# Performance work log

Hardware: AMD Instinct MI355X
Metric: run time of the kernel (lower is better)

The kernel has to match this reference:

```python
import jax, jax.numpy as jnp
import numpy as np

D_MODEL = 192   # embed_dim
DEPTH = 24
D_INNER = 384   # expand=2 * d_model
D_STATE = 16
D_CONV = 4
DT_RANK = 12    # ceil(192/16)
B = 8
IMG = 224
P = 16          # patch size / stride


def setup_inputs() -> dict:
    key = jax.random.key(0)
    ks = jax.random.split(key, 10)
    s = lambda k, shp, sc=0.02: jax.random.normal(k, shp, jnp.float32) * sc
    return {
        "x": jax.random.normal(ks[0], (B, 3, IMG, IMG), jnp.float32),
        "pe_w": s(ks[1], (D_MODEL, 3, P, P)),
        "pe_b": jnp.zeros((D_MODEL,), jnp.float32),
        "norm_w": jnp.ones((DEPTH, D_MODEL), jnp.float32),
        "norm_b": jnp.zeros((DEPTH, D_MODEL), jnp.float32),
        "in_proj_w": s(ks[2], (DEPTH, 2 * D_INNER, D_MODEL)),
        "conv_w": s(ks[3], (DEPTH, D_INNER, D_CONV), 0.1),
        "conv_b": jnp.zeros((DEPTH, D_INNER), jnp.float32),
        "xproj_w": s(ks[4], (DEPTH, DT_RANK + 2 * D_STATE, D_INNER)),
        "dtproj_w": s(ks[5], (DEPTH, D_INNER, DT_RANK), 0.1),
        "dtproj_b": s(ks[6], (DEPTH, D_INNER), 0.1),
        "A_log": jnp.broadcast_to(jnp.log(jnp.arange(1.0, D_STATE + 1.0, dtype=jnp.float32)), (DEPTH, D_INNER, D_STATE)).astype(jnp.float32),
        "D_param": jnp.ones((DEPTH, D_INNER), jnp.float32),
        "outproj_w": s(ks[7], (DEPTH, D_MODEL, D_INNER)),
        "normf_w": jnp.ones((D_MODEL,), jnp.float32),
        "normf_b": jnp.zeros((D_MODEL,), jnp.float32),
    }


def _layernorm(x, w, b, eps=1e-5):
    mu = x.mean(-1, keepdims=True)
    var = ((x - mu) ** 2).mean(-1, keepdims=True)
    return (x - mu) * jax.lax.rsqrt(var + eps) * w + b


def _causal_dwconv(x, w, b):
    # x: [B, L, d_inner]; depthwise causal conv1d (mamba conv1d, padding=d_conv-1, truncated to L)
    xt = jnp.pad(x.swapaxes(1, 2), ((0, 0), (0, 0), (D_CONV - 1, 0)))  # [B, di, L+3]
    y = jax.lax.conv_general_dilated(xt, w[:, None, :], (1,), 'VALID',
                                     feature_group_count=w.shape[0])
    return (y + b[:, None]).swapaxes(1, 2)  # [B, L, di]


def _selective_scan(u, dt, Bm, Cm, A, Dp):
    # u, dt: [B, L, di]; Bm, Cm: [B, L, ds]; A: [di, ds]; Dp: [di]
    dA = jnp.exp(dt[..., None] * A)                         # [B, L, di, ds]
    dBu = (dt * u)[..., None] * Bm[:, :, None, :]           # [B, L, di, ds]

    def step(h, inp):
        dA_t, dBu_t, C_t = inp
        h = dA_t * h + dBu_t                                # [B, di, ds]
        return h, jnp.einsum('bds,bs->bd', h, C_t)

    h0 = jnp.zeros((u.shape[0], A.shape[0], A.shape[1]), u.dtype)
    _, ys = jax.lax.scan(step, h0,
                         (dA.swapaxes(0, 1), dBu.swapaxes(0, 1), Cm.swapaxes(0, 1)))
    return ys.swapaxes(0, 1) + u * Dp                       # [B, L, di]


def _mamba(x, ipw, cw, cb, xpw, dtw, dtb, Alog, Dp, opw):
    xz = jnp.einsum('bld,ed->ble', x, ipw)                  # [B, L, 2*di]
    xin, z = jnp.split(xz, 2, axis=-1)
    xin = jax.nn.silu(_causal_dwconv(xin, cw, cb))
    xdbl = jnp.einsum('bld,ed->ble', xin, xpw)              # [B, L, dt_rank+2*ds]
    dt = jax.nn.softplus(jnp.einsum('blr,dr->bld', xdbl[..., :DT_RANK], dtw) + dtb)
    Bm = xdbl[..., DT_RANK:DT_RANK + D_STATE]
    Cm = xdbl[..., DT_RANK + D_STATE:]
    A = -jnp.exp(Alog)
    y = _selective_scan(xin, dt, Bm, Cm, A, Dp)
    y = y * jax.nn.silu(z)
    return jnp.einsum('bld,ed->ble', y, opw)                # [B, L, D]


def reference(x, pe_w, pe_b, norm_w, norm_b, in_proj_w, conv_w, conv_b,
              xproj_w, dtproj_w, dtproj_b, A_log, D_param, outproj_w,
              normf_w, normf_b):
    # PatchEmbed: conv stride 16 -> flatten -> [B, 196, 192]
    feat = jax.lax.conv_general_dilated(x, pe_w, (P, P), 'VALID') + pe_b[None, :, None, None]
    h = feat.reshape(feat.shape[0], D_MODEL, -1).swapaxes(1, 2)
    residual = None
    for i in range(DEPTH):
        residual = h if residual is None else residual + h
        hn = _layernorm(residual, norm_w[i], norm_b[i])
        h = _mamba(hn, in_proj_w[i], conv_w[i], conv_b[i], xproj_w[i],
                   dtproj_w[i], dtproj_b[i], A_log[i], D_param[i], outproj_w[i])
    residual = residual + h
    return _layernorm(residual, normf_w, normf_b)           # [B, 196, 192]
```

## Files before the change

### kernel.cpp

```cpp
#include <hip/hip_runtime.h>
#include <hip/hip_bf16.h>


#define NTOK   1568
#define DMODEL 192
#define DINNER 384
#define DSTATE 16
#define DTRANK 12
#define DEPTH  24
#define LSEQ   196
#define TCH    49
#define LDA    40

typedef __attribute__((ext_vector_type(8))) short short8;
typedef __attribute__((ext_vector_type(4))) short short4v;
typedef __attribute__((ext_vector_type(4))) float floatx4;

__device__ inline short f2bf(float f) {
    __hip_bfloat16 h = __float2bfloat16(f);
    return *reinterpret_cast<short*>(&h);
}

#define PR1 884736
#define PR2 1327104
#define PR3 1363968
#define PR4 1769472
#define PR5 1880064
#define PR6 3084288
__global__ __launch_bounds__(256) void prep(
    const float* __restrict__ inw, const float* __restrict__ outw,
    const float* __restrict__ pew, const float* __restrict__ xpw,
    const float* __restrict__ dtw, const float* __restrict__ x,
    short* __restrict__ w_in, short* __restrict__ w_out,
    short* __restrict__ w_pe, float* __restrict__ xpwT,
    float* __restrict__ dtwT, __hip_bfloat16* __restrict__ patches)
{
    int idx = blockIdx.x * 256 + threadIdx.x;
    if (idx < PR3) {
        float4 v; short* dst;
        if (idx < PR1)      { v = ((const float4*)inw)[idx];        dst = w_in  + (size_t)idx * 4; }
        else if (idx < PR2) { int i = idx - PR1; v = ((const float4*)outw)[i]; dst = w_out + (size_t)i * 4; }
        else                { int i = idx - PR2; v = ((const float4*)pew)[i];  dst = w_pe  + (size_t)i * 4; }
        short4v o;
        o[0] = f2bf(v.x); o[1] = f2bf(v.y); o[2] = f2bf(v.z); o[3] = f2bf(v.w);
        *(short4v*)dst = o;
    } else if (idx < PR4) {
        int i = idx - PR3;
        int layer = i / 16896, rem = i % 16896;
        int k = rem / 44, e = rem % 44;
        xpwT[i] = xpw[(size_t)layer * 16896 + e * 384 + k];
    } else if (idx < PR5) {
        int i = idx - PR4;
        int layer = i / 4608, rem = i % 4608;
        int r = rem / 384, d = rem % 384;
        dtwT[i] = dtw[(size_t)layer * 4608 + d * 12 + r];
    } else if (idx < PR6) {
        int i = idx - PR5;
        int tok = i / 768, e = i % 768;
        int b = tok / LSEQ, l = tok % LSEQ;
        int py = l / 14, px = l % 14;
        int ic = e >> 8, rem = e & 255, ky = rem >> 4, kx = rem & 15;
        patches[i] = __float2bfloat16(x[((b * 3 + ic) * 224 + py * 16 + ky) * 224 + px * 16 + kx]);
    }
}

template<int K>
__global__ __launch_bounds__(256) void gemm_in(
    const __hip_bfloat16* __restrict__ A, const short* __restrict__ Wb,
    float* __restrict__ C, int M, int N)
{
    __shared__ short As[64 * LDA];
    __shared__ short Ws[64 * LDA];
    int tid = threadIdx.x;
    int m0 = blockIdx.x * 64, n0 = blockIdx.y * 64;
    int wv = tid >> 6, lane = tid & 63;
    int fm = lane & 15, q = lane >> 4;
    int row = tid >> 2, kc = (tid & 3) * 8;
    const short* Ab = (const short*)A;
    floatx4 acc[4];
#pragma unroll
    for (int nt = 0; nt < 4; ++nt) acc[nt] = (floatx4){0.f, 0.f, 0.f, 0.f};

#pragma unroll
    for (int k0 = 0; k0 < K; k0 += 32) {
        {
            int m = m0 + row;
            short8 v = {0,0,0,0,0,0,0,0};
            if (m < M) v = *(const short8*)&Ab[(size_t)m * K + k0 + kc];
            *(short8*)&As[row * LDA + kc] = v;
        }
        {
            short8 w = *(const short8*)&Wb[(size_t)(n0 + row) * K + k0 + kc];
            *(short8*)&Ws[row * LDA + kc] = w;
        }
        __syncthreads();
        short8 af = *(const short8*)&As[(wv * 16 + fm) * LDA + q * 8];
#pragma unroll
        for (int nt = 0; nt < 4; ++nt) {
            short8 bf = *(const short8*)&Ws[(nt * 16 + fm) * LDA + q * 8];
            acc[nt] = __builtin_amdgcn_mfma_f32_16x16x32_bf16(af, bf, acc[nt], 0, 0, 0);
        }
        __syncthreads();
    }
#pragma unroll
    for (int nt = 0; nt < 4; ++nt) {
        int col = n0 + nt * 16 + fm;
#pragma unroll
        for (int r = 0; r < 4; ++r) {
            int mrow = m0 + wv * 16 + q * 4 + r;
            if (mrow < M) C[(size_t)mrow * N + col] = acc[nt][r];
        }
    }
}

template<int K>
__global__ __launch_bounds__(256) void gemm_ln(
    const __hip_bfloat16* __restrict__ A, const short* __restrict__ Wb,
    const float* __restrict__ bias, float* __restrict__ residual,
    __hip_bfloat16* __restrict__ hn, float* __restrict__ outf,
    const float* __restrict__ lnw, const float* __restrict__ lnb,
    int accumulate)
{
    __shared__ short As[16 * LDA];
    __shared__ short Ws[192 * LDA];
    __shared__ float slw[192], slb[192], sbias[192];
    __shared__ float sS1[4][16], sS2[4][16];
    int tid = threadIdx.x;
    int m0 = blockIdx.x * 16;
    int wv = tid >> 6, lane = tid & 63;
    int fm = lane & 15, q = lane >> 4;
    int wrow = tid >> 2, kc = (tid & 3) * 8;
    if (tid < 192) {
        slw[tid] = lnw[tid];
        slb[tid] = lnb[tid];
        sbias[tid] = bias ? bias[tid] : 0.f;
    }
    const short* Ab = (const short*)A;
    floatx4 acc[3];
#pragma unroll
    for (int j = 0; j < 3; ++j) acc[j] = (floatx4){0.f, 0.f, 0.f, 0.f};

    short8 aR = {0,0,0,0,0,0,0,0};
    short8 wR[3];
    if (tid < 64) aR = *(const short8*)&Ab[(size_t)(m0 + (tid >> 2)) * K + kc];
#pragma unroll
    for (int j = 0; j < 3; ++j)
        wR[j] = *(const short8*)&Wb[(size_t)(wrow + 64 * j) * K + kc];

// ... 39 lines not shown
        for (int j = 0; j < 3; ++j)
            residual[(size_t)m * DMODEL + (wv * 3 + j) * 16 + fm] = v[j][r];
    }
#pragma unroll
    for (int r = 0; r < 4; ++r) {
        float s1 = v[0][r] + v[1][r] + v[2][r];
        float s2 = v[0][r]*v[0][r] + v[1][r]*v[1][r] + v[2][r]*v[2][r];
        s1 += __shfl_xor(s1, 1); s2 += __shfl_xor(s2, 1);
        s1 += __shfl_xor(s1, 2); s2 += __shfl_xor(s2, 2);
        s1 += __shfl_xor(s1, 4); s2 += __shfl_xor(s2, 4);
        s1 += __shfl_xor(s1, 8); s2 += __shfl_xor(s2, 8);
        if (fm == 0) { sS1[wv][q * 4 + r] = s1; sS2[wv][q * 4 + r] = s2; }
    }
    __syncthreads();
#pragma unroll
    for (int r = 0; r < 4; ++r) {
        int row = q * 4 + r;
        int m = m0 + row;
        float S1 = sS1[0][row] + sS1[1][row] + sS1[2][row] + sS1[3][row];
        float S2 = sS2[0][row] + sS2[1][row] + sS2[2][row] + sS2[3][row];
        float mean = S1 * (1.f / DMODEL);
        float var  = S2 * (1.f / DMODEL) - mean * mean;
        float rstd = rsqrtf(var + 1e-5f);
#pragma unroll
        for (int j = 0; j < 3; ++j) {
            int col = (wv * 3 + j) * 16 + fm;
            float o = (v[j][r] - mean) * rstd * slw[col] + slb[col];
            if (outf) outf[(size_t)m * DMODEL + col] = o;
            else      hn[(size_t)m * DMODEL + col] = __float2bfloat16(o);
        }
    }
}

__global__ __launch_bounds__(256) void conv_xproj_dt(
    const float* __restrict__ xz, const float* __restrict__ cw,
    const float* __restrict__ cb, const float* __restrict__ xpwT,
    const float* __restrict__ dtwT, const float* __restrict__ dtb,
    float* __restrict__ u, float* __restrict__ dtg, float* __restrict__ bcg)
{
    __shared__ float sxz[7 * 384];
    __shared__ float su[4 * 384];
    __shared__ float sx[4 * 48];
    int blk = blockIdx.x;
    int b = blk / 49, c = blk % 49;
    int l0 = c * 4;
    int tid = threadIdx.x;

    for (int idx = tid; idx < 7 * 384; idx += 256) {
        int t = idx / 384, d = idx % 384;
        int l = l0 - 3 + t;
        sxz[idx] = (l >= 0) ? xz[(size_t)(b * LSEQ + l) * 768 + d] : 0.f;
    }
    __syncthreads();

    for (int idx = tid; idx < 4 * 384; idx += 256) {
        int t = idx / 384, d = idx % 384;
        float4 w4 = *(const float4*)&cw[d * 4];
        float acc = cb[d]
            + sxz[t * 384 + d]       * w4.x
            + sxz[(t + 1) * 384 + d] * w4.y
            + sxz[(t + 2) * 384 + d] * w4.z
            + sxz[(t + 3) * 384 + d] * w4.w;
        float sig = 1.f / (1.f + __expf(-acc));
        float val = acc * sig;
        su[idx] = val;
        u[(size_t)(b * LSEQ + l0 + t) * 384 + d] = val;
    }
    __syncthreads();

    {
        int wv = tid >> 6, e = tid & 63;
        if (e < 44) {
            float a0 = 0.f, a1 = 0.f, a2 = 0.f, a3 = 0.f;
            const float* ur = &su[wv * 384];
            for (int j = 0; j < 384; j += 4) {
                a0 += ur[j]     * xpwT[(j    ) * 44 + e];
                a1 += ur[j + 1] * xpwT[(j + 1) * 44 + e];
                a2 += ur[j + 2] * xpwT[(j + 2) * 44 + e];
                a3 += ur[j + 3] * xpwT[(j + 3) * 44 + e];
            }
            sx[wv * 48 + e] = (a0 + a1) + (a2 + a3);
        }
    }
    __syncthreads();

    for (int idx = tid; idx < 4 * 384; idx += 256) {
        int t = idx / 384, d = idx % 384;
        float acc = dtb[d];
#pragma unroll
        for (int r = 0; r < DTRANK; ++r) acc += sx[t * 48 + r] * dtwT[r * 384 + d];
        float sp = (acc > 20.f) ? acc : log1pf(__expf(acc));
        dtg[(size_t)(b * LSEQ + l0 + t) * 384 + d] = sp;
    }
    if (tid < 128) {
        int t = tid >> 5, j = tid & 31;
        bcg[(size_t)(b * LSEQ + l0 + t) * 32 + j] = sx[t * 48 + 12 + j];
    }
}

#define SPAD 272
__global__ __launch_bounds__(256) void scan_kernel(
    const float* __restrict__ u, const float* __restrict__ dtg,
    const float* __restrict__ bc, const float* __restrict__ xz,
    const float* __restrict__ Alog, const float* __restrict__ Dp,
    __hip_bfloat16* __restrict__ y)
{
    __shared__ float sdt[TCH][16];
    __shared__ float su_[TCH][16];
    __shared__ float sz_[TCH][16];
    __shared__ float sB_[TCH][16];
    __shared__ float sC_[TCH][16];
    __shared__ float sprod[TCH][SPAD];

    int b  = blockIdx.x / 24;
    int dg = blockIdx.x % 24;
    int tid = threadIdx.x;
    int s = tid & 15, dl = tid >> 4;
    int d = dg * 16 + dl;
    float Ads = -expf(Alog[d * DSTATE + s]);
    float Dd2 = Dp[dg * 16 + (tid & 15)];
    float h = 0.f;

    for (int c0 = 0; c0 < LSEQ; c0 += TCH) {
        if (tid < TCH * 4) {
            int t = tid >> 2, j4 = (tid & 3) * 4;
            size_t tok = (size_t)(b * LSEQ + c0 + t);
            *(float4*)&sdt[t][j4] = *(const float4*)&dtg[tok * DINNER + dg * 16 + j4];
            *(float4*)&su_[t][j4] = *(const float4*)&u  [tok * DINNER + dg * 16 + j4];
            *(float4*)&sz_[t][j4] = *(const float4*)&xz [tok * 768 + DINNER + dg * 16 + j4];
            *(float4*)&sB_[t][j4] = *(const float4*)&bc [tok * 32 + j4];
            *(float4*)&sC_[t][j4] = *(const float4*)&bc [tok * 32 + 16 + j4];
        }
        __syncthreads();

#pragma unroll 7
        for (int t = 0; t < TCH; ++t) {
            float dtv = sdt[t][dl];
            float uv  = su_[t][dl];
            float Bv  = sB_[t][s];
            float Cv  = sC_[t][s];
            float dA  = __expf(dtv * Ads);
            h = dA * h + (dtv * uv) * Bv;
            sprod[t][dl * 17 + s] = h * Cv;
        }
        __syncthreads();

        for (int i = tid; i < TCH * 16; i += 256) {
            int t = i >> 4, dl2 = i & 15;
            float sum = 0.f;
#pragma unroll
            for (int j = 0; j < 16; ++j) sum += sprod[t][dl2 * 17 + j];
            float uv = su_[t][dl2];
            float zv = sz_[t][dl2];
            float sig = 1.f / (1.f + __expf(-zv));
            y[(size_t)(b * LSEQ + c0 + t) * DINNER + dg * 16 + dl2] =
                __float2bfloat16((sum + uv * Dd2) * (zv * sig));
        }
        __syncthreads();
    }
}

extern "C" void kernel_launch(void* const* d_in, const int* in_sizes, int n_in,
                              void* d_out, int out_size, void* d_ws, size_t ws_size,
                              hipStream_t stream)
{
    const float* x         = (const float*)d_in[0];
    const float* pe_w      = (const float*)d_in[1];
    const float* pe_b      = (const float*)d_in[2];
    const float* norm_w    = (const float*)d_in[3];
    const float* norm_b    = (const float*)d_in[4];
    const float* in_proj_w = (const float*)d_in[5];
    const float* conv_w    = (const float*)d_in[6];
    const float* conv_b    = (const float*)d_in[7];
    const float* xproj_w   = (const float*)d_in[8];
    const float* dtproj_w  = (const float*)d_in[9];
    const float* dtproj_b  = (const float*)d_in[10];
    const float* A_log     = (const float*)d_in[11];
    const float* D_param   = (const float*)d_in[12];
    const float* outproj_w = (const float*)d_in[13];
    const float* normf_w   = (const float*)d_in[14];
    const float* normf_b   = (const float*)d_in[15];

    float* ws = (float*)d_ws;
    float* residual = ws;
    float* xz       = residual + 301056;
    float* ubuf     = xz + 1204224;
    float* dtbuf    = ubuf + 602112;
    float* bcbuf    = dtbuf + 602112;
    __hip_bfloat16* hn      = (__hip_bfloat16*)(ws + 2759680);
    __hip_bfloat16* ybf     = (__hip_bfloat16*)(ws + 2910208);
    __hip_bfloat16* patches = (__hip_bfloat16*)(ws + 3211264);
    short* w_in  = (short*)(ws + 3813376);
    short* w_out = (short*)(ws + 5582848);
    short* w_pe  = (short*)(ws + 6467584);
    float* xpwT  = ws + 6541312;
    float* dtwT  = xpwT + 405504;

    prep<<<12048, 256, 0, stream>>>(
        in_proj_w, outproj_w, pe_w, xproj_w, dtproj_w, x,
        w_in, w_out, w_pe, xpwT, dtwT, patches);
    gemm_ln<768><<<98, 256, 0, stream>>>(
        patches, w_pe, pe_b, residual, hn, nullptr, norm_w, norm_b, 0);

    for (int i = 0; i < DEPTH; ++i) {
        int last = (i == DEPTH - 1);
        gemm_in<192><<<dim3(25, 12), 256, 0, stream>>>(
            hn, w_in + (size_t)i * 768 * DMODEL, xz, NTOK, 768);
        conv_xproj_dt<<<392, 256, 0, stream>>>(
            xz, conv_w + (size_t)i * DINNER * 4, conv_b + (size_t)i * DINNER,
            xpwT + (size_t)i * 384 * 44, dtwT + (size_t)i * 12 * 384,
            dtproj_b + (size_t)i * DINNER, ubuf, dtbuf, bcbuf);
        scan_kernel<<<192, 256, 0, stream>>>(
            ubuf, dtbuf, bcbuf, xz, A_log + (size_t)i * DINNER * DSTATE,
            D_param + (size_t)i * DINNER, ybf);
        gemm_ln<384><<<98, 256, 0, stream>>>(
            ybf, w_out + (size_t)i * DMODEL * DINNER, nullptr, residual, hn,
            last ? (float*)d_out : nullptr,
            last ? normf_w : norm_w + (i + 1) * DMODEL,
            last ? normf_b : norm_b + (i + 1) * DMODEL,
            1);
    }
}
```

Before: 1.421 ms.

## Fuse all per-layer kernels into one persistent megakernel with grid barriers

Replaces the 96 per-layer launches (in-proj GEMM, conv/xproj/dt, scan, out-proj+LN) with a single persistent kernel of 512 blocks. Stages are separated by a hierarchical atomic grid barrier, and shared memory is a union of the per-stage layouts. The aim is to remove kernel launch overhead and inter-kernel gaps. The risks are barrier latency, lower occupancy from the two-blocks-per-CU bound, and deadlock if not all 512 blocks are co-resident, which is only partly guarded by a spin timeout.

```diff
diff --git a/kernel.cpp b/kernel.cpp
--- a/kernel.cpp
+++ b/kernel.cpp
@@ -11,6 +11,8 @@
 #define LSEQ   196
 #define TCH    49
 #define LDA    40
+#define SPAD   272
+#define NB     512
 
 typedef __attribute__((ext_vector_type(8))) short short8;
 typedef __attribute__((ext_vector_type(4))) short short4v;
@@ -19,6 +21,43 @@
 __device__ inline short f2bf(float f) {
     __hip_bfloat16 h = __float2bfloat16(f);
     return *reinterpret_cast<short*>(&h);
+}
+
+struct GiLDS { short As[64 * LDA]; short Ws[64 * LDA]; };
+struct CvLDS { float sxz[7 * 384]; float su[4 * 384]; float sx[4 * 48]; };
+struct ScLDS {
+    float sdt[TCH][16]; float su_[TCH][16]; float sz_[TCH][16];
+    float sB_[TCH][16]; float sC_[TCH][16]; float sprod[TCH][SPAD];
+};
+struct GlLDS {
+    short As[16 * LDA]; short Ws[192 * LDA];
+    float slw[192]; float slb[192]; float sS1[4][16]; float sS2[4][16];
+};
+union MegaLDS { GiLDS gi; CvLDS cv; ScLDS sc; GlLDS gl; };
+
+__device__ __forceinline__ void gridbar(unsigned* bar, unsigned eph) {
+    __syncthreads();
+    if (threadIdx.x == 0) {
+        unsigned g = (unsigned)blockIdx.x >> 3;
+        unsigned prev = __hip_atomic_fetch_add(&bar[32 + g * 16], 1u,
+                          __ATOMIC_ACQ_REL, __HIP_MEMORY_SCOPE_AGENT);
+        if (prev == (eph << 3) + 7u) {
+            unsigned rprev = __hip_atomic_fetch_add(&bar[16], 1u,
+                              __ATOMIC_ACQ_REL, __HIP_MEMORY_SCOPE_AGENT);
+            if (rprev == eph * (NB >> 3) + (NB >> 3) - 1u) {
+                __hip_atomic_store(&bar[0], eph + 1u,
+                    __ATOMIC_RELEASE, __HIP_MEMORY_SCOPE_AGENT);
+            }
+        }
+        unsigned tmo = 0;
+        while (__hip_atomic_load(&bar[0], __ATOMIC_RELAXED,
+                                 __HIP_MEMORY_SCOPE_AGENT) <= eph) {
+            __builtin_amdgcn_s_sleep(4);
+            if (++tmo > 100000u) break;
+        }
+        (void)__hip_atomic_load(&bar[0], __ATOMIC_ACQUIRE, __HIP_MEMORY_SCOPE_AGENT);
+    }
+    __syncthreads();
 }
 
 #define PR1 884736
@@ -27,13 +66,15 @@
 #define PR4 1769472
 #define PR5 1880064
 #define PR6 3084288
+#define PR7 3086336
 __global__ __launch_bounds__(256) void prep(
     const float* __restrict__ inw, const float* __restrict__ outw,
     const float* __restrict__ pew, const float* __restrict__ xpw,
     const float* __restrict__ dtw, const float* __restrict__ x,
     short* __restrict__ w_in, short* __restrict__ w_out,
     short* __restrict__ w_pe, float* __restrict__ xpwT,
-    float* __restrict__ dtwT, __hip_bfloat16* __restrict__ patches)
+    float* __restrict__ dtwT, __hip_bfloat16* __restrict__ patches,
+    unsigned* __restrict__ bar)
 {
     int idx = blockIdx.x * 256 + threadIdx.x;
     if (idx < PR3) {
@@ -61,55 +102,8 @@
         int py = l / 14, px = l % 14;
         int ic = e >> 8, rem = e & 255, ky = rem >> 4, kx = rem & 15;
         patches[i] = __float2bfloat16(x[((b * 3 + ic) * 224 + py * 16 + ky) * 224 + px * 16 + kx]);
-    }
-}
-
-template<int K>
-__global__ __launch_bounds__(256) void gemm_in(
-    const __hip_bfloat16* __restrict__ A, const short* __restrict__ Wb,
-    float* __restrict__ C, int M, int N)
-{
-    __shared__ short As[64 * LDA];
-    __shared__ short Ws[64 * LDA];
-    int tid = threadIdx.x;
-    int m0 = blockIdx.x * 64, n0 = blockIdx.y * 64;
-    int wv = tid >> 6, lane = tid & 63;
-    int fm = lane & 15, q = lane >> 4;
-    int row = tid >> 2, kc = (tid & 3) * 8;
-    const short* Ab = (const short*)A;
-    floatx4 acc[4];
-#pragma unroll
-    for (int nt = 0; nt < 4; ++nt) acc[nt] = (floatx4){0.f, 0.f, 0.f, 0.f};
-
-#pragma unroll
-    for (int k0 = 0; k0 < K; k0 += 32) {
-        {
-            int m = m0 + row;
-            short8 v = {0,0,0,0,0,0,0,0};
-            if (m < M) v = *(const short8*)&Ab[(size_t)m * K + k0 + kc];
-            *(short8*)&As[row * LDA + kc] = v;
-        }
-        {
-            short8 w = *(const short8*)&Wb[(size_t)(n0 + row) * K + k0 + kc];
-            *(short8*)&Ws[row * LDA + kc] = w;
-        }
-        __syncthreads();
-        short8 af = *(const short8*)&As[(wv * 16 + fm) * LDA + q * 8];
-#pragma unroll
-        for (int nt = 0; nt < 4; ++nt) {
-            short8 bf = *(const short8*)&Ws[(nt * 16 + fm) * LDA + q * 8];
-            acc[nt] = __builtin_amdgcn_mfma_f32_16x16x32_bf16(af, bf, acc[nt], 0, 0, 0);
-        }
-        __syncthreads();
-    }
-#pragma unroll
-    for (int nt = 0; nt < 4; ++nt) {
-        int col = n0 + nt * 16 + fm;
-#pragma unroll
-        for (int r = 0; r < 4; ++r) {
-            int mrow = m0 + wv * 16 + q * 4 + r;
-            if (mrow < M) C[(size_t)mrow * N + col] = acc[nt][r];
-        }
+    } else if (idx < PR7) {
+        bar[idx - PR6] = 0u;
     }
 }
 
@@ -219,131 +213,276 @@
     }
 }
 
-__global__ __launch_bounds__(256) void conv_xproj_dt(
-    const float* __restrict__ xz, const float* __restrict__ cw,
-    const float* __restrict__ cb, const float* __restrict__ xpwT,
-    const float* __restrict__ dtwT, const float* __restrict__ dtb,
-    float* __restrict__ u, float* __restrict__ dtg, float* __restrict__ bcg)
+__global__ __launch_bounds__(256, 2) void vim_mega(
+    const short* __restrict__ w_in, const float* __restrict__ conv_w,
+    const float* __restrict__ conv_b, const float* __restrict__ xpwT,
+    const float* __restrict__ dtwT, const float* __restrict__ dtb_all,
+    const float* __restrict__ A_log, const float* __restrict__ D_param,
+    const short* __restrict__ w_out, const float* __restrict__ norm_w,
+    const float* __restrict__ norm_b, const float* __restrict__ normf_w,
+    const float* __restrict__ normf_b, float* __restrict__ residual,
+    float* __restrict__ xz, float* __restrict__ ubuf,
+    float* __restrict__ dtbuf, float* __restrict__ bcbuf,
+    __hip_bfloat16* __restrict__ hn, __hip_bfloat16* __restrict__ ybf,
+    float* __restrict__ outF, unsigned* __restrict__ bar)
 {
-    __shared__ float sxz[7 * 384];
-    __shared__ float su[4 * 384];
-    __shared__ float sx[4 * 48];
-    int blk = blockIdx.x;
-    int b = blk / 49, c = blk % 49;
-    int l0 = c * 4;
+    __shared__ MegaLDS sm;
     int tid = threadIdx.x;
-
-    for (int idx = tid; idx < 7 * 384; idx += 256) {
-        int t = idx / 384, d = idx % 384;
-        int l = l0 - 3 + t;
-        sxz[idx] = (l >= 0) ? xz[(size_t)(b * LSEQ + l) * 768 + d] : 0.f;
-    }
-    __syncthreads();
-
-    for (int idx = tid; idx < 4 * 384; idx += 256) {
-        int t = idx / 384, d = idx % 384;
-        float4 w4 = *(const float4*)&cw[d * 4];
-        float acc = cb[d]
-            + sxz[t * 384 + d]       * w4.x
-            + sxz[(t + 1) * 384 + d] * w4.y
-            + sxz[(t + 2) * 384 + d] * w4.z
-            + sxz[(t + 3) * 384 + d] * w4.w;
-        float sig = 1.f / (1.f + __expf(-acc));
-        float val = acc * sig;
-        su[idx] = val;
-        u[(size_t)(b * LSEQ + l0 + t) * 384 + d] = val;
-    }
-    __syncthreads();
-
-    {
-        int wv = tid >> 6, e = tid & 63;
-        if (e < 44) {
-            float a0 = 0.f, a1 = 0.f, a2 = 0.f, a3 = 0.f;
-            const float* ur = &su[wv * 384];
-            for (int j = 0; j < 384; j += 4) {
-                a0 += ur[j]     * xpwT[(j    ) * 44 + e];
-                a1 += ur[j + 1] * xpwT[(j + 1) * 44 + e];
-                a2 += ur[j + 2] * xpwT[(j + 2) * 44 + e];
-                a3 += ur[j + 3] * xpwT[(j + 3) * 44 + e];
-            }
-            sx[wv * 48 + e] = (a0 + a1) + (a2 + a3);
-        }
-    }
-    __syncthreads();
-
-    for (int idx = tid; idx < 4 * 384; idx += 256) {
-        int t = idx / 384, d = idx % 384;
-        float acc = dtb[d];
-#pragma unroll
-        for (int r = 0; r < DTRANK; ++r) acc += sx[t * 48 + r] * dtwT[r * 384 + d];
-        float sp = (acc > 20.f) ? acc : log1pf(__expf(acc));
-        dtg[(size_t)(b * LSEQ + l0 + t) * 384 + d] = sp;
-    }
-    if (tid < 128) {
-        int t = tid >> 5, j = tid & 31;
-        bcg[(size_t)(b * LSEQ + l0 + t) * 32 + j] = sx[t * 48 + 12 + j];
-    }
-}
-
-#define SPAD 272
-__global__ __launch_bounds__(256) void scan_kernel(
-    const float* __restrict__ u, const float* __restrict__ dtg,
-    const float* __restrict__ bc, const float* __restrict__ xz,
-    const float* __restrict__ Alog, const float* __restrict__ Dp,
-    __hip_bfloat16* __restrict__ y)
-{
-    __shared__ float sdt[TCH][16];
-    __shared__ float su_[TCH][16];
-    __shared__ float sz_[TCH][16];
-    __shared__ float sB_[TCH][16];
-    __shared__ float sC_[TCH][16];
-    __shared__ float sprod[TCH][SPAD];
-
-    int b  = blockIdx.x / 24;
-    int dg = blockIdx.x % 24;
-    int tid = threadIdx.x;
-    int s = tid & 15, dl = tid >> 4;
-    int d = dg * 16 + dl;
-    float Ads = -expf(Alog[d * DSTATE + s]);
-    float Dd2 = Dp[dg * 16 + (tid & 15)];
-    float h = 0.f;
-
-    for (int c0 = 0; c0 < LSEQ; c0 += TCH) {
-        if (tid < TCH * 4) {
-            int t = tid >> 2, j4 = (tid & 3) * 4;
-            size_t tok = (size_t)(b * LSEQ + c0 + t);
-            *(float4*)&sdt[t][j4] = *(const float4*)&dtg[tok * DINNER + dg * 16 + j4];
-            *(float4*)&su_[t][j4] = *(const float4*)&u  [tok * DINNER + dg * 16 + j4];
-            *(float4*)&sz_[t][j4] = *(const float4*)&xz [tok * 768 + DINNER + dg * 16 + j4];
-            *(float4*)&sB_[t][j4] = *(const float4*)&bc [tok * 32 + j4];
-            *(float4*)&sC_[t][j4] = *(const float4*)&bc [tok * 32 + 16 + j4];
-        }
-        __syncthreads();
+    unsigned eph = 0;
+
+    for (int L = 0; L < DEPTH; ++L) {
+        if (blockIdx.x < 300) {
+            const short* wi = w_in + (size_t)L * 768 * DMODEL;
+            int m0 = (blockIdx.x / 12) * 64, n0 = (blockIdx.x % 12) * 64;
+            int wv = tid >> 6, lane = tid & 63;
+            int fm = lane & 15, q = lane >> 4;
+            int row = tid >> 2, kc = (tid & 3) * 8;
+            const short* Ab = (const short*)hn;
+            floatx4 acc[4];
+#pragma unroll
+            for (int nt = 0; nt < 4; ++nt) acc[nt] = (floatx4){0.f, 0.f, 0.f, 0.f};
+#pragma unroll
+            for (int k0 = 0; k0 < DMODEL; k0 += 32) {
+                {
+                    int m = m0 + row;
+                    short8 v = {0,0,0,0,0,0,0,0};
+                    if (m < NTOK) v = *(const short8*)&Ab[(size_t)m * DMODEL + k0 + kc];
+                    *(short8*)&sm.gi.As[row * LDA + kc] = v;
+                }
+                {
+                    short8 w = *(const short8*)&wi[(size_t)(n0 + row) * DMODEL + k0 + kc];
+                    *(short8*)&sm.gi.Ws[row * LDA + kc] = w;
+                }
+                __syncthreads();
+                short8 af = *(const short8*)&sm.gi.As[(wv * 16 + fm) * LDA + q * 8];
+#pragma unroll
+                for (int nt = 0; nt < 4; ++nt) {
+                    short8 bf = *(const short8*)&sm.gi.Ws[(nt * 16 + fm) * LDA + q * 8];
+                    acc[nt] = __builtin_amdgcn_mfma_f32_16x16x32_bf16(af, bf, acc[nt], 0, 0, 0);
+                }
+                __syncthreads();
+            }
+#pragma unroll
+            for (int nt = 0; nt < 4; ++nt) {
+                int col = n0 + nt * 16 + fm;
+#pragma unroll
+                for (int r = 0; r < 4; ++r) {
+                    int mrow = m0 + wv * 16 + q * 4 + r;
+                    if (mrow < NTOK) xz[(size_t)mrow * 768 + col] = acc[nt][r];
+                }
+            }
+        }
+        gridbar(bar, eph); ++eph;
+
+        if (blockIdx.x < 392) {
+            const float* cw   = conv_w  + (size_t)L * DINNER * 4;
+            const float* cb   = conv_b  + (size_t)L * DINNER;
+            const float* xpwl = xpwT    + (size_t)L * 384 * 44;
+            const float* dtwl = dtwT    + (size_t)L * 12 * 384;
+            const float* dtb  = dtb_all + (size_t)L * DINNER;
+            int b = blockIdx.x / 49, c = blockIdx.x % 49;
+            int l0 = c * 4;
+
+            for (int idx = tid; idx < 7 * 384; idx += 256) {
+                int t = idx / 384, d = idx % 384;
+                int l = l0 - 3 + t;
+                sm.cv.sxz[idx] = (l >= 0) ? xz[(size_t)(b * LSEQ + l) * 768 + d] : 0.f;
+            }
+            __syncthreads();
+
+            for (int idx = tid; idx < 4 * 384; idx += 256) {
+                int t = idx / 384, d = idx % 384;
+                float4 w4 = *(const float4*)&cw[d * 4];
+                float acc = cb[d]
+                    + sm.cv.sxz[t * 384 + d]       * w4.x
+                    + sm.cv.sxz[(t + 1) * 384 + d] * w4.y
+                    + sm.cv.sxz[(t + 2) * 384 + d] * w4.z
+                    + sm.cv.sxz[(t + 3) * 384 + d] * w4.w;
+                float sig = 1.f / (1.f + __expf(-acc));
+                float val = acc * sig;
+                sm.cv.su[idx] = val;
+                ubuf[(size_t)(b * LSEQ + l0 + t) * 384 + d] = val;
+            }
+            __syncthreads();
+
+            {
+                int wv = tid >> 6, e = tid & 63;
+                if (e < 44) {
+                    float a0 = 0.f, a1 = 0.f, a2 = 0.f, a3 = 0.f;
+                    const float* ur = &sm.cv.su[wv * 384];
+                    for (int j = 0; j < 384; j += 4) {
+                        a0 += ur[j]     * xpwl[(j    ) * 44 + e];
+                        a1 += ur[j + 1] * xpwl[(j + 1) * 44 + e];
+                        a2 += ur[j + 2] * xpwl[(j + 2) * 44 + e];
+                        a3 += ur[j + 3] * xpwl[(j + 3) * 44 + e];
+                    }
+                    sm.cv.sx[wv * 48 + e] = (a0 + a1) + (a2 + a3);
+                }
+            }
+            __syncthreads();
+
+            for (int idx = tid; idx < 4 * 384; idx += 256) {
+                int t = idx / 384, d = idx % 384;
+                float acc = dtb[d];
+#pragma unroll
+                for (int r = 0; r < DTRANK; ++r) acc += sm.cv.sx[t * 48 + r] * dtwl[r * 384 + d];
+                float sp = (acc > 20.f) ? acc : log1pf(__expf(acc));
+                dtbuf[(size_t)(b * LSEQ + l0 + t) * 384 + d] = sp;
+            }
+            if (tid < 128) {
+                int t = tid >> 5, j = tid & 31;
+                bcbuf[(size_t)(b * LSEQ + l0 + t) * 32 + j] = sm.cv.sx[t * 48 + 12 + j];
+            }
+        }
+        gridbar(bar, eph); ++eph;
+
+        if (blockIdx.x < 192) {
+            const float* Al = A_log + (size_t)L * DINNER * DSTATE;
+            const float* Dl = D_param + (size_t)L * DINNER;
+            int b  = blockIdx.x / 24;
+            int dg = blockIdx.x % 24;
+            int s = tid & 15, dl = tid >> 4;
+            int d = dg * 16 + dl;
+            float Ads = -expf(Al[d * DSTATE + s]);
+            float Dd2 = Dl[dg * 16 + (tid & 15)];
+            float h = 0.f;
+
+            for (int c0 = 0; c0 < LSEQ; c0 += TCH) {
+                if (tid < TCH * 4) {
+                    int t = tid >> 2, j4 = (tid & 3) * 4;
+                    size_t tok = (size_t)(b * LSEQ + c0 + t);
+                    *(float4*)&sm.sc.sdt[t][j4] = *(const float4*)&dtbuf[tok * DINNER + dg * 16 + j4];
+                    *(float4*)&sm.sc.su_[t][j4] = *(const float4*)&ubuf [tok * DINNER + dg * 16 + j4];
+                    *(float4*)&sm.sc.sz_[t][j4] = *(const float4*)&xz   [tok * 768 + DINNER + dg * 16 + j4];
+                    *(float4*)&sm.sc.sB_[t][j4] = *(const float4*)&bcbuf[tok * 32 + j4];
+                    *(float4*)&sm.sc.sC_[t][j4] = *(const float4*)&bcbuf[tok * 32 + 16 + j4];
+                }
+                __syncthreads();
 
 #pragma unroll 7
-        for (int t = 0; t < TCH; ++t) {
-            float dtv = sdt[t][dl];
-            float uv  = su_[t][dl];
-            float Bv  = sB_[t][s];
-            float Cv  = sC_[t][s];
-            float dA  = __expf(dtv * Ads);
-            h = dA * h + (dtv * uv) * Bv;
-            sprod[t][dl * 17 + s] = h * Cv;
-        }
-        __syncthreads();
-
-        for (int i = tid; i < TCH * 16; i += 256) {
-            int t = i >> 4, dl2 = i & 15;
-            float sum = 0.f;
-#pragma unroll
-            for (int j = 0; j < 16; ++j) sum += sprod[t][dl2 * 17 + j];
-            float uv = su_[t][dl2];
-            float zv = sz_[t][dl2];
-            float sig = 1.f / (1.f + __expf(-zv));
-            y[(size_t)(b * LSEQ + c0 + t) * DINNER + dg * 16 + dl2] =
-                __float2bfloat16((sum + uv * Dd2) * (zv * sig));
-        }
-        __syncthreads();
+                for (int t = 0; t < TCH; ++t) {
+                    float dtv = sm.sc.sdt[t][dl];
+                    float uv  = sm.sc.su_[t][dl];
+                    float Bv  = sm.sc.sB_[t][s];
+                    float Cv  = sm.sc.sC_[t][s];
+                    float dA  = __expf(dtv * Ads);
+                    h = dA * h + (dtv * uv) * Bv;
+                    sm.sc.sprod[t][dl * 17 + s] = h * Cv;
+                }
+                __syncthreads();
+
+                for (int i = tid; i < TCH * 16; i += 256) {
+                    int t = i >> 4, dl2 = i & 15;
+                    float sum = 0.f;
+#pragma unroll
+                    for (int j = 0; j < 16; ++j) sum += sm.sc.sprod[t][dl2 * 17 + j];
+                    float uv = sm.sc.su_[t][dl2];
+                    float zv = sm.sc.sz_[t][dl2];
+                    float sig = 1.f / (1.f + __expf(-zv));
+                    ybf[(size_t)(b * LSEQ + c0 + t) * DINNER + dg * 16 + dl2] =
+                        __float2bfloat16((sum + uv * Dd2) * (zv * sig));
+                }
+                __syncthreads();
+            }
+        }
+        gridbar(bar, eph); ++eph;
+
+        if (blockIdx.x < 98) {
+            int last = (L == DEPTH - 1);
+            const float* lnw = last ? normf_w : norm_w + (size_t)(L + 1) * DMODEL;
+            const float* lnb = last ? normf_b : norm_b + (size_t)(L + 1) * DMODEL;
+            const short* Wb  = w_out + (size_t)L * DMODEL * DINNER;
+            float* outf = last ? outF : nullptr;
+            int m0 = blockIdx.x * 16;
+            int wv = tid >> 6, lane = tid & 63;
+            int fm = lane & 15, q = lane >> 4;
+            int wrow = tid >> 2, kc = (tid & 3) * 8;
+            if (tid < 192) {
+                sm.gl.slw[tid] = lnw[tid];
+                sm.gl.slb[tid] = lnb[tid];
+            }
+            const short* Ab = (const short*)ybf;
+            floatx4 acc[3];
+#pragma unroll
+            for (int j = 0; j < 3; ++j) acc[j] = (floatx4){0.f, 0.f, 0.f, 0.f};
+
+            short8 aR = {0,0,0,0,0,0,0,0};
+            short8 wR[3];
+            if (tid < 64) aR = *(const short8*)&Ab[(size_t)(m0 + (tid >> 2)) * DINNER + kc];
+#pragma unroll
+            for (int j = 0; j < 3; ++j)
+                wR[j] = *(const short8*)&Wb[(size_t)(wrow + 64 * j) * DINNER + kc];
+
+            for (int k0 = 0; k0 < DINNER; k0 += 32) {
+                if (tid < 64) *(short8*)&sm.gl.As[(tid >> 2) * LDA + kc] = aR;
+#pragma unroll
+                for (int j = 0; j < 3; ++j)
+                    *(short8*)&sm.gl.Ws[(wrow + 64 * j) * LDA + kc] = wR[j];
+                __syncthreads();
+                int kn = k0 + 32;
+                if (kn < DINNER) {
+                    if (tid < 64) aR = *(const short8*)&Ab[(size_t)(m0 + (tid >> 2)) * DINNER + kn + kc];
+#pragma unroll
+                    for (int j = 0; j < 3; ++j)
+                        wR[j] = *(const short8*)&Wb[(size_t)(wrow + 64 * j) * DINNER + kn + kc];
+                }
+                short8 af = *(const short8*)&sm.gl.As[fm * LDA + q * 8];
+#pragma unroll
+                for (int j = 0; j < 3; ++j) {
+                    int ct = wv * 3 + j;
+                    short8 bf = *(const short8*)&sm.gl.Ws[(ct * 16 + fm) * LDA + q * 8];
+                    acc[j] = __builtin_amdgcn_mfma_f32_16x16x32_bf16(af, bf, acc[j], 0, 0, 0);
+                }
+                __syncthreads();
+            }
+
+            float v[3][4];
+#pragma unroll
+            for (int r = 0; r < 4; ++r) {
+                int m = m0 + q * 4 + r;
+#pragma unroll
+                for (int j = 0; j < 3; ++j) {
+                    int col = (wv * 3 + j) * 16 + fm;
+                    v[j][r] = acc[j][r] + residual[(size_t)m * DMODEL + col];
+                }
+            }
+#pragma unroll
+            for (int r = 0; r < 4; ++r) {
+                int m = m0 + q * 4 + r;
+#pragma unroll
+                for (int j = 0; j < 3; ++j)
+                    residual[(size_t)m * DMODEL + (wv * 3 + j) * 16 + fm] = v[j][r];
+            }
+#pragma unroll
+            for (int r = 0; r < 4; ++r) {
+                float s1 = v[0][r] + v[1][r] + v[2][r];
+                float s2 = v[0][r]*v[0][r] + v[1][r]*v[1][r] + v[2][r]*v[2][r];
+                s1 += __shfl_xor(s1, 1); s2 += __shfl_xor(s2, 1);
+                s1 += __shfl_xor(s1, 2); s2 += __shfl_xor(s2, 2);
+                s1 += __shfl_xor(s1, 4); s2 += __shfl_xor(s2, 4);
+                s1 += __shfl_xor(s1, 8); s2 += __shfl_xor(s2, 8);
+                if (fm == 0) { sm.gl.sS1[wv][q * 4 + r] = s1; sm.gl.sS2[wv][q * 4 + r] = s2; }
+            }
+            __syncthreads();
+#pragma unroll
+            for (int r = 0; r < 4; ++r) {
+                int row = q * 4 + r;
+                int m = m0 + row;
+                float S1 = sm.gl.sS1[0][row] + sm.gl.sS1[1][row] + sm.gl.sS1[2][row] + sm.gl.sS1[3][row];
+                float S2 = sm.gl.sS2[0][row] + sm.gl.sS2[1][row] + sm.gl.sS2[2][row] + sm.gl.sS2[3][row];
+                float mean = S1 * (1.f / DMODEL);
+                float var  = S2 * (1.f / DMODEL) - mean * mean;
+                float rstd = rsqrtf(var + 1e-5f);
+#pragma unroll
+                for (int j = 0; j < 3; ++j) {
+                    int col = (wv * 3 + j) * 16 + fm;
+                    float o = (v[j][r] - mean) * rstd * sm.gl.slw[col] + sm.gl.slb[col];
+                    if (outf) outf[(size_t)m * DMODEL + col] = o;
+                    else      hn[(size_t)m * DMODEL + col] = __float2bfloat16(o);
+                }
+            }
+        }
+        gridbar(bar, eph); ++eph;
     }
 }
 
@@ -382,29 +521,15 @@
     short* w_pe  = (short*)(ws + 6467584);
     float* xpwT  = ws + 6541312;
     float* dtwT  = xpwT + 405504;
-
-    prep<<<12048, 256, 0, stream>>>(
+    unsigned* bar = (unsigned*)(ws + 7057408);
+
+    prep<<<12056, 256, 0, stream>>>(
         in_proj_w, outproj_w, pe_w, xproj_w, dtproj_w, x,
-        w_in, w_out, w_pe, xpwT, dtwT, patches);
+        w_in, w_out, w_pe, xpwT, dtwT, patches, bar);
     gemm_ln<768><<<98, 256, 0, stream>>>(
         patches, w_pe, pe_b, residual, hn, nullptr, norm_w, norm_b, 0);
-
-    for (int i = 0; i < DEPTH; ++i) {
-        int last = (i == DEPTH - 1);
-        gemm_in<192><<<dim3(25, 12), 256, 0, stream>>>(
-            hn, w_in + (size_t)i * 768 * DMODEL, xz, NTOK, 768);
-        conv_xproj_dt<<<392, 256, 0, stream>>>(
-            xz, conv_w + (size_t)i * DINNER * 4, conv_b + (size_t)i * DINNER,
-            xpwT + (size_t)i * 384 * 44, dtwT + (size_t)i * 12 * 384,
-            dtproj_b + (size_t)i * DINNER, ubuf, dtbuf, bcbuf);
-        scan_kernel<<<192, 256, 0, stream>>>(
-            ubuf, dtbuf, bcbuf, xz, A_log + (size_t)i * DINNER * DSTATE,
-            D_param + (size_t)i * DINNER, ybf);
-        gemm_ln<384><<<98, 256, 0, stream>>>(
-            ybf, w_out + (size_t)i * DMODEL * DINNER, nullptr, residual, hn,
-            last ? (float*)d_out : nullptr,
-            last ? normf_w : norm_w + (i + 1) * DMODEL,
-            last ? normf_b : norm_b + (i + 1) * DMODEL,
-            1);
-    }
+    vim_mega<<<NB, 256, 0, stream>>>(
+        w_in, conv_w, conv_b, xpwT, dtwT, dtproj_b, A_log, D_param, w_out,
+        norm_w, norm_b, normf_w, normf_b, residual, xz, ubuf, dtbuf, bcbuf,
+        hn, ybf, (float*)d_out, bar);
 }
```

New measurement: 3.780 ms. 166% more time.

## Fuse in-projection GEMM with causal conv, x-proj and dt-proj per token block

Applied to the files above, without the earlier changes.

Merges the in_proj GEMM into the conv/x-proj/dt kernel. Each block computes 8 tokens plus a 3-token causal halo via MFMA, keeps the x half in shared memory and writes only the z half to a compact buffer. This removes one launch per layer and the full xz round trip through global memory. In exchange, each of the 196 blocks reloads the whole 768x192 weight and recomputes 3 halo rows, and the conv now masks taps by sequence position across batch boundaries.

```diff
diff --git a/kernel.cpp b/kernel.cpp
--- a/kernel.cpp
+++ b/kernel.cpp
@@ -11,6 +11,8 @@
 #define LSEQ   196
 #define TCH    49
 #define LDA    40
+#define ALD    200
+#define SPAD   272
 
 typedef __attribute__((ext_vector_type(8))) short short8;
 typedef __attribute__((ext_vector_type(4))) short short4v;
@@ -65,55 +67,6 @@
 }
 
 template<int K>
-__global__ __launch_bounds__(256) void gemm_in(
-    const __hip_bfloat16* __restrict__ A, const short* __restrict__ Wb,
-    float* __restrict__ C, int M, int N)
-{
-    __shared__ short As[64 * LDA];
-    __shared__ short Ws[64 * LDA];
-    int tid = threadIdx.x;
-    int m0 = blockIdx.x * 64, n0 = blockIdx.y * 64;
-    int wv = tid >> 6, lane = tid & 63;
-    int fm = lane & 15, q = lane >> 4;
-    int row = tid >> 2, kc = (tid & 3) * 8;
-    const short* Ab = (const short*)A;
-    floatx4 acc[4];
-#pragma unroll
-    for (int nt = 0; nt < 4; ++nt) acc[nt] = (floatx4){0.f, 0.f, 0.f, 0.f};
-
-#pragma unroll
-    for (int k0 = 0; k0 < K; k0 += 32) {
-        {
-            int m = m0 + row;
-            short8 v = {0,0,0,0,0,0,0,0};
-            if (m < M) v = *(const short8*)&Ab[(size_t)m * K + k0 + kc];
-            *(short8*)&As[row * LDA + kc] = v;
-        }
-        {
-            short8 w = *(const short8*)&Wb[(size_t)(n0 + row) * K + k0 + kc];
-            *(short8*)&Ws[row * LDA + kc] = w;
-        }
-        __syncthreads();
-        short8 af = *(const short8*)&As[(wv * 16 + fm) * LDA + q * 8];
-#pragma unroll
-        for (int nt = 0; nt < 4; ++nt) {
-            short8 bf = *(const short8*)&Ws[(nt * 16 + fm) * LDA + q * 8];
-            acc[nt] = __builtin_amdgcn_mfma_f32_16x16x32_bf16(af, bf, acc[nt], 0, 0, 0);
-        }
-        __syncthreads();
-    }
-#pragma unroll
-    for (int nt = 0; nt < 4; ++nt) {
-        int col = n0 + nt * 16 + fm;
-#pragma unroll
-        for (int r = 0; r < 4; ++r) {
-            int mrow = m0 + wv * 16 + q * 4 + r;
-            if (mrow < M) C[(size_t)mrow * N + col] = acc[nt][r];
-        }
-    }
-}
-
-template<int K>
 __global__ __launch_bounds__(256) void gemm_ln(
     const __hip_bfloat16* __restrict__ A, const short* __restrict__ Wb,
     const float* __restrict__ bias, float* __restrict__ residual,
@@ -219,76 +172,120 @@
     }
 }
 
-__global__ __launch_bounds__(256) void conv_xproj_dt(
-    const float* __restrict__ xz, const float* __restrict__ cw,
-    const float* __restrict__ cb, const float* __restrict__ xpwT,
-    const float* __restrict__ dtwT, const float* __restrict__ dtb,
+struct FaEpi { float sxin[12 * 384]; float su[8 * 384]; float sx[8 * 48]; };
+union FaU { short Ws[768 * LDA]; FaEpi e; };
+
+__global__ __launch_bounds__(256) void in_conv_xproj(
+    const __hip_bfloat16* __restrict__ hn, const short* __restrict__ wi,
+    const float* __restrict__ cw, const float* __restrict__ cb,
+    const float* __restrict__ xpwl, const float* __restrict__ dtwl,
+    const float* __restrict__ dtb, float* __restrict__ zbuf,
     float* __restrict__ u, float* __restrict__ dtg, float* __restrict__ bcg)
 {
-    __shared__ float sxz[7 * 384];
-    __shared__ float su[4 * 384];
-    __shared__ float sx[4 * 48];
-    int blk = blockIdx.x;
-    int b = blk / 49, c = blk % 49;
-    int l0 = c * 4;
+    __shared__ short As[16 * ALD];
+    __shared__ FaU sm;
     int tid = threadIdx.x;
-
-    for (int idx = tid; idx < 7 * 384; idx += 256) {
+    int g0 = blockIdx.x * 8;
+    int wv = tid >> 6, lane = tid & 63;
+    int fm = lane & 15, q = lane >> 4;
+
+    const short* Ab = (const short*)hn;
+    for (int idx = tid; idx < 16 * 24; idx += 256) {
+        int row = idx / 24, kc8 = (idx % 24) * 8;
+        int ar = g0 - 3 + row;
+        short8 v = {0,0,0,0,0,0,0,0};
+        if (row < 11 && ar >= 0) v = *(const short8*)&Ab[(size_t)ar * DMODEL + kc8];
+        *(short8*)&As[row * ALD + kc8] = v;
+    }
+
+    floatx4 acc[12];
+#pragma unroll
+    for (int j = 0; j < 12; ++j) acc[j] = (floatx4){0.f, 0.f, 0.f, 0.f};
+
+    for (int k0 = 0; k0 < DMODEL; k0 += 32) {
+        for (int idx = tid; idx < 768 * 4; idx += 256) {
+            int n = idx >> 2, kc = (idx & 3) * 8;
+            *(short8*)&sm.Ws[n * LDA + kc] = *(const short8*)&wi[(size_t)n * DMODEL + k0 + kc];
+        }
+        __syncthreads();
+        short8 af = *(const short8*)&As[fm * ALD + k0 + q * 8];
+#pragma unroll
+        for (int j = 0; j < 12; ++j) {
+            short8 bf = *(const short8*)&sm.Ws[((wv * 12 + j) * 16 + fm) * LDA + q * 8];
+            acc[j] = __builtin_amdgcn_mfma_f32_16x16x32_bf16(af, bf, acc[j], 0, 0, 0);
+        }
+        __syncthreads();
+    }
+
+#pragma unroll
+    for (int j = 0; j < 12; ++j) {
+        int col = wv * 192 + j * 16 + fm;
+#pragma unroll
+        for (int r = 0; r < 4; ++r) {
+            int row = q * 4 + r;
+            float val = acc[j][r];
+            if (col < 384) {
+                if (row < 11) sm.e.sxin[row * 384 + col] = val;
+            } else {
+                int t = row - 3;
+                if (t >= 0 && t < 8) zbuf[(size_t)(g0 + t) * 384 + (col - 384)] = val;
+            }
+        }
+    }
+    __syncthreads();
+
+    for (int idx = tid; idx < 8 * 384; idx += 256) {
         int t = idx / 384, d = idx % 384;
-        int l = l0 - 3 + t;
-        sxz[idx] = (l >= 0) ? xz[(size_t)(b * LSEQ + l) * 768 + d] : 0.f;
+        int l = (g0 + t) % LSEQ;
+        float4 w4 = *(const float4*)&cw[d * 4];
+        float a = cb[d] + sm.e.sxin[(t + 3) * 384 + d] * w4.w;
+        if (l >= 1) a += sm.e.sxin[(t + 2) * 384 + d] * w4.z;
+        if (l >= 2) a += sm.e.sxin[(t + 1) * 384 + d] * w4.y;
+        if (l >= 3) a += sm.e.sxin[(t    ) * 384 + d] * w4.x;
+        float sig = 1.f / (1.f + __expf(-a));
+        float val = a * sig;
+        sm.e.su[idx] = val;
+        u[(size_t)(g0 + t) * 384 + d] = val;
     }
     __syncthreads();
 
-    for (int idx = tid; idx < 4 * 384; idx += 256) {
+    {
+        int e_ = tid & 63;
+        if (e_ < 44) {
+#pragma unroll
+            for (int half = 0; half < 2; ++half) {
+                int t = wv + half * 4;
+                const float* ur = &sm.e.su[t * 384];
+                float a0 = 0.f, a1 = 0.f, a2 = 0.f, a3 = 0.f;
+                for (int jj = 0; jj < 384; jj += 4) {
+                    a0 += ur[jj]     * xpwl[(jj    ) * 44 + e_];
+                    a1 += ur[jj + 1] * xpwl[(jj + 1) * 44 + e_];
+                    a2 += ur[jj + 2] * xpwl[(jj + 2) * 44 + e_];
+                    a3 += ur[jj + 3] * xpwl[(jj + 3) * 44 + e_];
+                }
+                sm.e.sx[t * 48 + e_] = (a0 + a1) + (a2 + a3);
+            }
+        }
+    }
+    __syncthreads();
+
+    for (int idx = tid; idx < 8 * 384; idx += 256) {
         int t = idx / 384, d = idx % 384;
-        float4 w4 = *(const float4*)&cw[d * 4];
-        float acc = cb[d]
-            + sxz[t * 384 + d]       * w4.x
-            + sxz[(t + 1) * 384 + d] * w4.y
-            + sxz[(t + 2) * 384 + d] * w4.z
-            + sxz[(t + 3) * 384 + d] * w4.w;
-        float sig = 1.f / (1.f + __expf(-acc));
-        float val = acc * sig;
-        su[idx] = val;
-        u[(size_t)(b * LSEQ + l0 + t) * 384 + d] = val;
-    }
-    __syncthreads();
-
+        float a = dtb[d];
+#pragma unroll
+        for (int r = 0; r < DTRANK; ++r) a += sm.e.sx[t * 48 + r] * dtwl[r * 384 + d];
+        float sp = (a > 20.f) ? a : log1pf(__expf(a));
+        dtg[(size_t)(g0 + t) * 384 + d] = sp;
+    }
     {
-        int wv = tid >> 6, e = tid & 63;
-        if (e < 44) {
-            float a0 = 0.f, a1 = 0.f, a2 = 0.f, a3 = 0.f;
-            const float* ur = &su[wv * 384];
-            for (int j = 0; j < 384; j += 4) {
-                a0 += ur[j]     * xpwT[(j    ) * 44 + e];
-                a1 += ur[j + 1] * xpwT[(j + 1) * 44 + e];
-                a2 += ur[j + 2] * xpwT[(j + 2) * 44 + e];
-                a3 += ur[j + 3] * xpwT[(j + 3) * 44 + e];
-            }
-            sx[wv * 48 + e] = (a0 + a1) + (a2 + a3);
-        }
-    }
-    __syncthreads();
-
-    for (int idx = tid; idx < 4 * 384; idx += 256) {
-        int t = idx / 384, d = idx % 384;
-        float acc = dtb[d];
-#pragma unroll
-        for (int r = 0; r < DTRANK; ++r) acc += sx[t * 48 + r] * dtwT[r * 384 + d];
-        float sp = (acc > 20.f) ? acc : log1pf(__expf(acc));
-        dtg[(size_t)(b * LSEQ + l0 + t) * 384 + d] = sp;
-    }
-    if (tid < 128) {
         int t = tid >> 5, j = tid & 31;
-        bcg[(size_t)(b * LSEQ + l0 + t) * 32 + j] = sx[t * 48 + 12 + j];
-    }
-}
-
-#define SPAD 272
+        bcg[(size_t)(g0 + t) * 32 + j] = sm.e.sx[t * 48 + 12 + j];
+    }
+}
+
 __global__ __launch_bounds__(256) void scan_kernel(
     const float* __restrict__ u, const float* __restrict__ dtg,
-    const float* __restrict__ bc, const float* __restrict__ xz,
+    const float* __restrict__ bc, const float* __restrict__ zbuf,
     const float* __restrict__ Alog, const float* __restrict__ Dp,
     __hip_bfloat16* __restrict__ y)
 {
@@ -312,11 +309,11 @@
         if (tid < TCH * 4) {
             int t = tid >> 2, j4 = (tid & 3) * 4;
             size_t tok = (size_t)(b * LSEQ + c0 + t);
-            *(float4*)&sdt[t][j4] = *(const float4*)&dtg[tok * DINNER + dg * 16 + j4];
-            *(float4*)&su_[t][j4] = *(const float4*)&u  [tok * DINNER + dg * 16 + j4];
-            *(float4*)&sz_[t][j4] = *(const float4*)&xz [tok * 768 + DINNER + dg * 16 + j4];
-            *(float4*)&sB_[t][j4] = *(const float4*)&bc [tok * 32 + j4];
-            *(float4*)&sC_[t][j4] = *(const float4*)&bc [tok * 32 + 16 + j4];
+            *(float4*)&sdt[t][j4] = *(const float4*)&dtg [tok * DINNER + dg * 16 + j4];
+            *(float4*)&su_[t][j4] = *(const float4*)&u   [tok * DINNER + dg * 16 + j4];
+            *(float4*)&sz_[t][j4] = *(const float4*)&zbuf[tok * DINNER + dg * 16 + j4];
+            *(float4*)&sB_[t][j4] = *(const float4*)&bc  [tok * 32 + j4];
+            *(float4*)&sC_[t][j4] = *(const float4*)&bc  [tok * 32 + 16 + j4];
         }
         __syncthreads();
 
@@ -370,8 +367,8 @@
 
     float* ws = (float*)d_ws;
     float* residual = ws;
-    float* xz       = residual + 301056;
-    float* ubuf     = xz + 1204224;
+    float* zbuf     = residual + 301056;
+    float* ubuf     = zbuf + 602112;
     float* dtbuf    = ubuf + 602112;
     float* bcbuf    = dtbuf + 602112;
     __hip_bfloat16* hn      = (__hip_bfloat16*)(ws + 2759680);
@@ -391,14 +388,13 @@
 
     for (int i = 0; i < DEPTH; ++i) {
         int last = (i == DEPTH - 1);
-        gemm_in<192><<<dim3(25, 12), 256, 0, stream>>>(
-            hn, w_in + (size_t)i * 768 * DMODEL, xz, NTOK, 768);
-        conv_xproj_dt<<<392, 256, 0, stream>>>(
-            xz, conv_w + (size_t)i * DINNER * 4, conv_b + (size_t)i * DINNER,
+        in_conv_xproj<<<196, 256, 0, stream>>>(
+            hn, w_in + (size_t)i * 768 * DMODEL,
+            conv_w + (size_t)i * DINNER * 4, conv_b + (size_t)i * DINNER,
             xpwT + (size_t)i * 384 * 44, dtwT + (size_t)i * 12 * 384,
-            dtproj_b + (size_t)i * DINNER, ubuf, dtbuf, bcbuf);
+            dtproj_b + (size_t)i * DINNER, zbuf, ubuf, dtbuf, bcbuf);
         scan_kernel<<<192, 256, 0, stream>>>(
-            ubuf, dtbuf, bcbuf, xz, A_log + (size_t)i * DINNER * DSTATE,
+            ubuf, dtbuf, bcbuf, zbuf, A_log + (size_t)i * DINNER * DSTATE,
             D_param + (size_t)i * DINNER, ybf);
         gemm_ln<384><<<98, 256, 0, stream>>>(
             ybf, w_out + (size_t)i * DMODEL * DINNER, nullptr, residual, hn,
```

New measurement: 1.916 ms. 34.8% more time.

## Reduce scan state products with DPP row sums and transpose scan smem

Applied to the files above, without the earlier changes.

Rewrites the selective-scan kernel so the 16-way reduction over state dimensions uses DPP cross-lane adds within each 16-lane row instead of writing every h*C product to a large shared array and summing afterwards. Per-chunk inputs are stored transposed in shared memory so each thread can read four timesteps at once as float4. This removes the large sprod buffer and its second-pass reduction, at the cost of DPP latency on the serial recurrence path and scalar, uncoalesced transposed global loads.

```diff
diff --git a/kernel.cpp b/kernel.cpp
--- a/kernel.cpp
+++ b/kernel.cpp
@@ -10,6 +10,7 @@
 #define DEPTH  24
 #define LSEQ   196
 #define TCH    49
+#define TPAD   52
 #define LDA    40
 
 typedef __attribute__((ext_vector_type(8))) short short8;
@@ -19,6 +20,20 @@
 __device__ inline short f2bf(float f) {
     __hip_bfloat16 h = __float2bfloat16(f);
     return *reinterpret_cast<short*>(&h);
+}
+
+__device__ __forceinline__ float rowsum16(float x) {
+    float v = x;
+    int i;
+    i = __builtin_amdgcn_mov_dpp(__float_as_int(v), 0xB1, 0xf, 0xf, false);
+    v += __int_as_float(i);
+    i = __builtin_amdgcn_mov_dpp(__float_as_int(v), 0x4E, 0xf, 0xf, false);
+    v += __int_as_float(i);
+    i = __builtin_amdgcn_mov_dpp(__float_as_int(v), 0x124, 0xf, 0xf, false);
+    v += __int_as_float(i);
+    i = __builtin_amdgcn_mov_dpp(__float_as_int(v), 0x128, 0xf, 0xf, false);
+    v += __int_as_float(i);
+    return v;
 }
 
 #define PR1 884736
@@ -285,66 +300,77 @@
     }
 }
 
-#define SPAD 272
 __global__ __launch_bounds__(256) void scan_kernel(
     const float* __restrict__ u, const float* __restrict__ dtg,
     const float* __restrict__ bc, const float* __restrict__ xz,
     const float* __restrict__ Alog, const float* __restrict__ Dp,
     __hip_bfloat16* __restrict__ y)
 {
-    __shared__ float sdt[TCH][16];
-    __shared__ float su_[TCH][16];
-    __shared__ float sz_[TCH][16];
-    __shared__ float sB_[TCH][16];
-    __shared__ float sC_[TCH][16];
-    __shared__ float sprod[TCH][SPAD];
+    __shared__ float sdtT[16][TPAD];
+    __shared__ float suT [16][TPAD];
+    __shared__ float szT [16][TPAD];
+    __shared__ float sBT [16][TPAD];
+    __shared__ float sCT [16][TPAD];
+    __shared__ float sy  [TCH][16];
 
     int b  = blockIdx.x / 24;
     int dg = blockIdx.x % 24;
     int tid = threadIdx.x;
-    int s = tid & 15, dl = tid >> 4;
-    int d = dg * 16 + dl;
-    float Ads = -expf(Alog[d * DSTATE + s]);
-    float Dd2 = Dp[dg * 16 + (tid & 15)];
+    int s = tid & 15, dch = tid >> 4;
+    float Ads = -expf(Alog[(dg * 16 + dch) * DSTATE + s]);
+    float Dd  = Dp[dg * 16 + (tid & 15)];
     float h = 0.f;
 
+#define SCAN_STEP(dtv, uv, Bv, Cv, tt)                      \
+    {                                                       \
+        float dA = __expf((dtv) * Ads);                     \
+        h = dA * h + ((dtv) * (uv)) * (Bv);                 \
+        float p = rowsum16(h * (Cv));                       \
+        if (s == 0) sy[tt][dch] = p;                        \
+    }
+
     for (int c0 = 0; c0 < LSEQ; c0 += TCH) {
-        if (tid < TCH * 4) {
-            int t = tid >> 2, j4 = (tid & 3) * 4;
+        for (int idx = tid; idx < TCH * 16; idx += 256) {
+            int t = idx >> 4, j = idx & 15;
             size_t tok = (size_t)(b * LSEQ + c0 + t);
-            *(float4*)&sdt[t][j4] = *(const float4*)&dtg[tok * DINNER + dg * 16 + j4];
-            *(float4*)&su_[t][j4] = *(const float4*)&u  [tok * DINNER + dg * 16 + j4];
-            *(float4*)&sz_[t][j4] = *(const float4*)&xz [tok * 768 + DINNER + dg * 16 + j4];
-            *(float4*)&sB_[t][j4] = *(const float4*)&bc [tok * 32 + j4];
-            *(float4*)&sC_[t][j4] = *(const float4*)&bc [tok * 32 + 16 + j4];
-        }
-        __syncthreads();
-
-#pragma unroll 7
-        for (int t = 0; t < TCH; ++t) {
-            float dtv = sdt[t][dl];
-            float uv  = su_[t][dl];
-            float Bv  = sB_[t][s];
-            float Cv  = sC_[t][s];
-            float dA  = __expf(dtv * Ads);
-            h = dA * h + (dtv * uv) * Bv;
-            sprod[t][dl * 17 + s] = h * Cv;
-        }
-        __syncthreads();
-
-        for (int i = tid; i < TCH * 16; i += 256) {
-            int t = i >> 4, dl2 = i & 15;
-            float sum = 0.f;
-#pragma unroll
-            for (int j = 0; j < 16; ++j) sum += sprod[t][dl2 * 17 + j];
-            float uv = su_[t][dl2];
-            float zv = sz_[t][dl2];
+            sdtT[j][t] = dtg[tok * DINNER + dg * 16 + j];
+            suT [j][t] = u  [tok * DINNER + dg * 16 + j];
+            szT [j][t] = xz [tok * 768 + DINNER + dg * 16 + j];
+            sBT [j][t] = bc [tok * 32 + j];
+            sCT [j][t] = bc [tok * 32 + 16 + j];
+        }
+        __syncthreads();
+
+        for (int t4 = 0; t4 < TCH - 1; t4 += 4) {
+            float4 dt4 = *(const float4*)&sdtT[dch][t4];
+            float4 u4  = *(const float4*)&suT [dch][t4];
+            float4 B4  = *(const float4*)&sBT [s][t4];
+            float4 C4  = *(const float4*)&sCT [s][t4];
+            SCAN_STEP(dt4.x, u4.x, B4.x, C4.x, t4 + 0)
+            SCAN_STEP(dt4.y, u4.y, B4.y, C4.y, t4 + 1)
+            SCAN_STEP(dt4.z, u4.z, B4.z, C4.z, t4 + 2)
+            SCAN_STEP(dt4.w, u4.w, B4.w, C4.w, t4 + 3)
+        }
+        {
+            int t = TCH - 1;
+            float dtv = sdtT[dch][t], uv = suT[dch][t];
+            float Bv = sBT[s][t],     Cv = sCT[s][t];
+            SCAN_STEP(dtv, uv, Bv, Cv, t)
+        }
+        __syncthreads();
+
+        for (int idx = tid; idx < TCH * 16; idx += 256) {
+            int t = idx >> 4, c = idx & 15;
+            float sum = sy[t][c];
+            float uv = suT[c][t];
+            float zv = szT[c][t];
             float sig = 1.f / (1.f + __expf(-zv));
-            y[(size_t)(b * LSEQ + c0 + t) * DINNER + dg * 16 + dl2] =
-                __float2bfloat16((sum + uv * Dd2) * (zv * sig));
-        }
-        __syncthreads();
-    }
+            y[(size_t)(b * LSEQ + c0 + t) * DINNER + dg * 16 + c] =
+                __float2bfloat16((sum + uv * Dd) * (zv * sig));
+        }
+        __syncthreads();
+    }
+#undef SCAN_STEP
 }
 
 extern "C" void kernel_launch(void* const* d_in, const int* in_sizes, int n_in,
```

After: 1.615 ms. +13.7%, slower.
